# Kernel optimization log

Measured on AMD Instinct MI355X. Metric: run time of the kernel, lower is better.

The kernel has to match this reference:

```python
import jax, jax.numpy as jnp
import numpy as np

HEADS = 8
DIM_HEAD = 64
SCALE = DIM_HEAD ** -0.5


def setup_inputs() -> dict:
    key = jax.random.key(0)
    ks = jax.random.split(key, 6)
    B, S, D = 4, 2048, 512
    return {
        "hidden_states": jax.random.normal(ks[0], (B, S, D), jnp.float32),
        "Wq": jax.random.normal(ks[1], (D, D), jnp.float32) * (D ** -0.5),
        "Wk": jax.random.normal(ks[2], (D, D), jnp.float32) * (D ** -0.5),
        "Wv": jax.random.normal(ks[3], (D, D), jnp.float32) * (D ** -0.5),
        "Wo": jax.random.normal(ks[4], (D, D), jnp.float32) * (D ** -0.5),
        "bo": jnp.zeros((D,), jnp.float32),
    }


def reference(hidden_states, Wq, Wk, Wv, Wo, bo):
    B, S, D = hidden_states.shape
    H, Dh = HEADS, DIM_HEAD
    # Linear projections (torch Linear: x @ W.T; weights here stored as [D, D] used directly)
    q = hidden_states @ Wq  # [B,S,D]
    k = hidden_states @ Wk
    v = hidden_states @ Wv
    # head_to_batch_dim: [B,S,D] -> [B,H,S,Dh]
    q = q.reshape(B, S, H, Dh).transpose(0, 2, 1, 3)
    k = k.reshape(B, S, H, Dh).transpose(0, 2, 1, 3)
    v = v.reshape(B, S, H, Dh).transpose(0, 2, 1, 3)
    # scaled dot-product attention, scores materialized as in baddbmm path
    scores = jnp.einsum("bhqd,bhkd->bhqk", q, k) * SCALE  # [B,H,S,S]
    probs = jax.nn.softmax(scores, axis=-1)
    out = jnp.einsum("bhqk,bhkd->bhqd", probs, v)  # [B,H,S,Dh]
    # batch_to_head_dim: [B,H,S,Dh] -> [B,S,D]
    out = out.transpose(0, 2, 1, 3).reshape(B, S, D)
    # output projection (Dropout with p=0 is identity)
    return out @ Wo + bo
```

## Files before the change

kernel.cpp:

```cpp
#include <hip/hip_runtime.h>
#include <cstdint>
#include <cstddef>


typedef __bf16 bf16;
typedef __bf16 bf16x4_t __attribute__((ext_vector_type(4)));
typedef __bf16 bf16x8_t __attribute__((ext_vector_type(8)));
typedef float  floatx4  __attribute__((ext_vector_type(4)));
typedef short  shortx4  __attribute__((ext_vector_type(4)));
typedef uint32_t u32x4  __attribute__((ext_vector_type(4)));

#define NB   4
#define SEQ  2048
#define DM   512
#define NH   8
#define DH   64
#define MTOT (NB * SEQ)


__device__ __forceinline__ void gload16(const void* g, void* l) {
    __builtin_amdgcn_global_load_lds((const __attribute__((address_space(1))) unsigned int*)g,
                                     (__attribute__((address_space(3))) unsigned int*)l,
                                     16, 0, 0);
}

__device__ __forceinline__ shortx4 pack4(floatx4 v) {
    union { bf16x4_t h; shortx4 s; } u;
    u.h = (bf16x4_t){ (bf16)v[0], (bf16)v[1], (bf16)v[2], (bf16)v[3] };
    return u.s;
}

__global__ __launch_bounds__(256) void prep(
        const float* __restrict__ X, const float* __restrict__ Wq, const float* __restrict__ Wk,
        const float* __restrict__ Wv, const float* __restrict__ Wo,
        bf16* __restrict__ xb, bf16* __restrict__ Wqkvt, bf16* __restrict__ Wot) {
    __shared__ float T[64][65];
    const int tid = threadIdx.x;
    const int bx = blockIdx.x;
    if (bx < 4096) {
        int i = (bx * 256 + tid) * 4;
        float4 v = *(const float4*)(X + i);
        bf16x4_t o = { (bf16)v.x, (bf16)v.y, (bf16)v.z, (bf16)v.w };
        *(bf16x4_t*)(xb + i) = o;
        return;
    }
    const int idx = bx - 4096;
    const int m = idx >> 6;
    const int k0 = ((idx >> 3) & 7) * 64, n0 = (idx & 7) * 64;
    const float* W = (m == 0) ? Wq : (m == 1) ? Wk : (m == 2) ? Wv : Wo;
    const float scale = (m == 0) ? 0.18033688011112042f : 1.0f;
#pragma unroll
    for (int p = 0; p < 4; p++) {
        int row = p * 16 + (tid >> 4), col = (tid & 15) * 4;
        float4 v = *(const float4*)(W + (size_t)(k0 + row) * DM + n0 + col);
        T[row][col + 0] = v.x * scale; T[row][col + 1] = v.y * scale;
        T[row][col + 2] = v.z * scale; T[row][col + 3] = v.w * scale;
    }
    __syncthreads();
#pragma unroll
    for (int p = 0; p < 4; p++) {
        int nr = p * 16 + (tid >> 4), kc = (tid & 15) * 4;
        bf16x4_t o = { (bf16)T[kc][nr], (bf16)T[kc + 1][nr], (bf16)T[kc + 2][nr], (bf16)T[kc + 3][nr] };
        bf16* dst = (m < 3) ? (Wqkvt + ((size_t)(m * DM + n0 + nr)) * DM + k0 + kc)
                            : (Wot + (size_t)(n0 + nr) * DM + k0 + kc);
        *(bf16x4_t*)dst = o;
    }
}

__global__ __launch_bounds__(256) void gemm_qkv(
        const bf16* __restrict__ A, const bf16* __restrict__ Bt,
        bf16* __restrict__ Qh, bf16* __restrict__ Kh, bf16* __restrict__ Vt) {
    __shared__ __attribute__((aligned(16))) bf16 AB[2][2][128 * 64];
    const int tid = threadIdx.x;
    const int wave = tid >> 6, lane = tid & 63;
    const int l15 = lane & 15, quad = lane >> 4, h7 = l15 & 7;
    const int m0 = blockIdx.x * 128, n0 = blockIdx.y * 128;
    const int mw = (wave >> 1) * 64, nw = (wave & 1) * 64;
    const int srow = lane >> 3, sc = (lane & 7) ^ srow;

    auto stage = [&](int buf, int k0) {
#pragma unroll
        for (int t = 0; t < 4; t++) {
            int rb = wave * 32 + t * 8;
            gload16(A  + (size_t)(m0 + rb + srow) * DM + k0 + sc * 8, AB[buf][0] + rb * 64);
            gload16(Bt + (size_t)(n0 + rb + srow) * DM + k0 + sc * 8, AB[buf][1] + rb * 64);
        }
    };

    floatx4 zero = {0.f, 0.f, 0.f, 0.f};
    floatx4 acc[4][4];
#pragma unroll
    for (int i = 0; i < 4; i++)
#pragma unroll
        for (int j = 0; j < 4; j++) acc[i][j] = zero;

    stage(0, 0);
    for (int kt = 0; kt < DM / 64; kt++) {
        __syncthreads();
        if (kt + 1 < DM / 64) stage((kt + 1) & 1, (kt + 1) * 64);
        const bf16* As = AB[kt & 1][0];
        const bf16* Bs = AB[kt & 1][1];
#pragma unroll
        for (int ks = 0; ks < 2; ks++) {
            bf16x8_t af[4], bfr[4];
#pragma unroll
            for (int i = 0; i < 4; i++)
                af[i] = *(const bf16x8_t*)(As + (mw + i * 16 + l15) * 64 + (((ks * 4 + quad) ^ h7) * 8));
#pragma unroll
            for (int j = 0; j < 4; j++)
                bfr[j] = *(const bf16x8_t*)(Bs + (nw + j * 16 + l15) * 64 + (((ks * 4 + quad) ^ h7) * 8));
#pragma unroll
            for (int i = 0; i < 4; i++)
#pragma unroll
                for (int j = 0; j < 4; j++)
                    acc[i][j] = __builtin_amdgcn_mfma_f32_16x16x32_bf16(af[i], bfr[j], acc[i][j], 0, 0, 0);
        }
    }

    bf16* E = (bf16*)AB;
    const int sect = n0 >> 9;
    const int bq = m0 >> 11;
    __syncthreads();
    if (sect != 2) {
        bf16* dstbase = (sect == 0) ? Qh : Kh;
#pragma unroll
        for (int i = 0; i < 4; i++)
#pragma unroll
            for (int j = 0; j < 4; j++)
#pragma unroll
                for (int r = 0; r < 4; r++)
                    E[(mw + i * 16 + quad * 4 + r) * 136 + nw + j * 16 + l15] = (bf16)acc[i][j][r];
        __syncthreads();
#pragma unroll
        for (int pp = 0; pp < 8; pp++) {
            int idx = pp * 256 + tid;
            int rowl = idx >> 4, chunk = idx & 15;
            u32x4 v = *(const u32x4*)(E + rowl * 136 + chunk * 8);
            int s = (m0 + rowl) & (SEQ - 1);
            int n = n0 + chunk * 8;
            int h = (n >> 6) & 7, d = n & 63;
            *(u32x4*)(dstbase + (((size_t)(bq * NH + h)) * SEQ + s) * DH + d) = v;
        }
    } else {
#pragma unroll
        for (int i = 0; i < 4; i++)
#pragma unroll
            for (int j = 0; j < 4; j++)
                *(shortx4*)(E + (nw + j * 16 + l15) * 136 + mw + i * 16 + quad * 4) = pack4(acc[i][j]);
        __syncthreads();
#pragma unroll
        for (int pp = 0; pp < 8; pp++) {
            int idx = pp * 256 + tid;
            int rowl = idx >> 4, chunk = idx & 15;
            u32x4 v = *(const u32x4*)(E + rowl * 136 + chunk * 8);
            int n = n0 + rowl;
            int h = (n >> 6) & 7, d = n & 63;
            int s = (m0 & (SEQ - 1)) + chunk * 8;
            *(u32x4*)(Vt + (((size_t)(bq * NH + h)) * DH + d) * SEQ + s) = v;
        }
    }
}

__global__ __launch_bounds__(256) void gemm_out(
        const bf16* __restrict__ A, const bf16* __restrict__ Bt,
        const float* __restrict__ bo, float* __restrict__ out) {
    __shared__ __attribute__((aligned(16))) bf16 Ao[2][64 * 64];
    __shared__ __attribute__((aligned(16))) bf16 Bo[2][128 * 64];
    const int tid = threadIdx.x;
    const int wave = tid >> 6, lane = tid & 63;
    const int l15 = lane & 15, quad = lane >> 4, h7 = l15 & 7;
    const int m0 = blockIdx.x * 64, n0 = blockIdx.y * 128;
    const int nw = wave * 32;
    const int srow = lane >> 3, sc = (lane & 7) ^ srow;

    auto stage = [&](int buf, int k0) {
#pragma unroll
        for (int t = 0; t < 2; t++) {
            int rb = wave * 16 + t * 8;
            gload16(A + (size_t)(m0 + rb + srow) * DM + k0 + sc * 8, Ao[buf] + rb * 64);
        }
#pragma unroll
        for (int t = 0; t < 4; t++) {
            int rb = wave * 32 + t * 8;
            gload16(Bt + (size_t)(n0 + rb + srow) * DM + k0 + sc * 8, Bo[buf] + rb * 64);
        }
    };

    floatx4 zero = {0.f, 0.f, 0.f, 0.f};
    floatx4 acc[4][2];
#pragma unroll
    for (int i = 0; i < 4; i++)
#pragma unroll
        for (int j = 0; j < 2; j++) acc[i][j] = zero;

    stage(0, 0);
    for (int kt = 0; kt < DM / 64; kt++) {
        __syncthreads();
        if (kt + 1 < DM / 64) stage((kt + 1) & 1, (kt + 1) * 64);
        const bf16* As = Ao[kt & 1];
        const bf16* Bs = Bo[kt & 1];
#pragma unroll
        for (int ks = 0; ks < 2; ks++) {
            bf16x8_t af[4], bfr[2];
#pragma unroll
            for (int i = 0; i < 4; i++)
                af[i] = *(const bf16x8_t*)(As + (i * 16 + l15) * 64 + (((ks * 4 + quad) ^ h7) * 8));
#pragma unroll
            for (int j = 0; j < 2; j++)
                bfr[j] = *(const bf16x8_t*)(Bs + (nw + j * 16 + l15) * 64 + (((ks * 4 + quad) ^ h7) * 8));
#pragma unroll
            for (int i = 0; i < 4; i++)
#pragma unroll
                for (int j = 0; j < 2; j++)
                    acc[i][j] = __builtin_amdgcn_mfma_f32_16x16x32_bf16(af[i], bfr[j], acc[i][j], 0, 0, 0);
        }
    }
#pragma unroll
    for (int i = 0; i < 4; i++)
#pragma unroll
        for (int j = 0; j < 2; j++)
#pragma unroll
            for (int r = 0; r < 4; r++) {
                int m = m0 + i * 16 + quad * 4 + r;
                int n = n0 + nw + j * 16 + l15;
                out[(size_t)m * DM + n] = acc[i][j][r] + bo[n];
            }
}

__global__ __launch_bounds__(256, 2) void flash_attn(
        const bf16* __restrict__ Q, const bf16* __restrict__ Kh,
        const bf16* __restrict__ Vt, bf16* __restrict__ Ob) {
    __shared__ __attribute__((aligned(16))) bf16 SMEM[4 * 8192];
    const int tid = threadIdx.x;
    const int wave = tid >> 6, lane = tid & 63;
    const int l15 = lane & 15, quad = lane >> 4, h7 = l15 & 7;
    const int qh = wave >> 1, kvh = wave & 1;
    const int qt = blockIdx.x & 15, bh = blockIdx.x >> 4;
    const int q0 = qt * 128;
    const bf16* Kb = Kh + (size_t)bh * SEQ * DH;
    const bf16* Vb = Vt + (size_t)bh * DH * SEQ;

    bf16x8_t aq[4][2];
#pragma unroll
    for (int sub = 0; sub < 4; sub++) {
        const bf16* qr = Q + ((size_t)bh * SEQ + q0 + qh * 64 + sub * 16 + l15) * DH;
        aq[sub][0] = *(const bf16x8_t*)(qr + quad * 8);
        aq[sub][1] = *(const bf16x8_t*)(qr + 32 + quad * 8);
    }

    const int srow = lane >> 3, sc = (lane & 7) ^ srow;
    auto stage = [&](int buf, int kv0) {
#pragma unroll
        for (int t = 0; t < 2; t++) {
            int rb = wave * 16 + t * 8;
            gload16(Kb + (size_t)(kv0 + rb + srow) * DH + sc * 8, SMEM + buf * 8192 + rb * 64);
            gload16(Vb + (size_t)(rb + srow) * SEQ + kv0 + sc * 8, SMEM + buf * 8192 + 4096 + rb * 64);
        }
    };

    floatx4 zero = {0.f, 0.f, 0.f, 0.f};
    floatx4 oacc[4][4];
    float l_run[4] = {0.f, 0.f, 0.f, 0.f};
#pragma unroll
    for (int sub = 0; sub < 4; sub++)
#pragma unroll
        for (int d = 0; d < 4; d++) oacc[sub][d] = zero;

    stage(0, 0);
    stage(1, 64);
    for (int seg = 0; seg < 16; seg++) {
        __syncthreads();
        if (seg < 15) {
            stage((2 * seg + 2) & 3, (2 * seg + 2) * 64);
            stage((2 * seg + 3) & 3, (2 * seg + 3) * 64);
        }
#pragma unroll
        for (int half = 0; half < 2; half++) {
            const bf16* Ks = SMEM + ((2 * seg + half) & 3) * 8192;
            const bf16* Vs = Ks + 4096;
            floatx4 st[4][2];
#pragma unroll
            for (int nsl = 0; nsl < 2; nsl++) {
                int row = (kvh * 2 + nsl) * 16 + l15;
                const bf16* kr = Ks + row * 64;
                bf16x8_t k0 = *(const bf16x8_t*)(kr + ((quad ^ h7) * 8));
                bf16x8_t k1 = *(const bf16x8_t*)(kr + (((4 + quad) ^ h7) * 8));
#pragma unroll
                for (int sub = 0; sub < 4; sub++) {
                    floatx4 a = zero;
                    a = __builtin_amdgcn_mfma_f32_16x16x32_bf16(k0, aq[sub][0], a, 0, 0, 0);
                    a = __builtin_amdgcn_mfma_f32_16x16x32_bf16(k1, aq[sub][1], a, 0, 0, 0);
                    st[sub][nsl] = a;
                }
            }
#pragma unroll
            for (int sub = 0; sub < 4; sub++) {
                float s = 0.f;
#pragma unroll
                for (int nsl = 0; nsl < 2; nsl++)
#pragma unroll
                    for (int r = 0; r < 4; r++) {
                        float p = __builtin_amdgcn_exp2f(st[sub][nsl][r]);
                        st[sub][nsl][r] = p;
                        s += p;
                    }
                l_run[sub] += s;
            }
#pragma unroll
            for (int cl = 0; cl < 2; cl++) {
                int c = kvh * 2 + cl;
                shortx4 ap[4];
#pragma unroll
                for (int sub = 0; sub < 4; sub++) ap[sub] = pack4(st[sub][cl]);
                int cc = 2 * c + (quad >> 1);
#pragma unroll
                for (int d = 0; d < 4; d++) {
                    const bf16* vr = Vs + (d * 16 + l15) * 64;
                    shortx4 bv = *(const shortx4*)(vr + ((cc ^ h7) * 8) + (quad & 1) * 4);
#pragma unroll
                    for (int sub = 0; sub < 4; sub++)
                        oacc[sub][d] = __builtin_amdgcn_mfma_f32_16x16x16bf16_1k(ap[sub], bv, oacc[sub][d], 0, 0, 0);
                }
            }
        }
    }

    float lf[4];
#pragma unroll
    for (int sub = 0; sub < 4; sub++) {
        float l = l_run[sub];
        l += __shfl_xor(l, 16, 64);
        l += __shfl_xor(l, 32, 64);
        lf[sub] = l;
    }
    __syncthreads();
    float* blob = (float*)SMEM + qh * (68 * 64);
    if (kvh == 1) {
#pragma unroll
        for (int sub = 0; sub < 4; sub++)
#pragma unroll
            for (int d = 0; d < 4; d++)
#pragma unroll
                for (int r = 0; r < 4; r++)
                    blob[((sub * 4 + d) * 4 + r) * 64 + lane] = oacc[sub][d][r];
#pragma unroll
        for (int sub = 0; sub < 4; sub++)
            blob[(64 + sub) * 64 + lane] = lf[sub];
    }
    __syncthreads();
    if (kvh == 0) {
#pragma unroll
        for (int sub = 0; sub < 4; sub++)
#pragma unroll
            for (int d = 0; d < 4; d++)
#pragma unroll
                for (int r = 0; r < 4; r++)
                    oacc[sub][d][r] += blob[((sub * 4 + d) * 4 + r) * 64 + lane];
#pragma unroll
        for (int sub = 0; sub < 4; sub++)
            lf[sub] += blob[(64 + sub) * 64 + lane];

        const int b = bh >> 3, h = bh & 7;
#pragma unroll
        for (int sub = 0; sub < 4; sub++) {
            float linv[4];
#pragma unroll
            for (int r = 0; r < 4; r++) linv[r] = 1.0f / __shfl(lf[sub], quad * 4 + r, 64);
#pragma unroll
            for (int d = 0; d < 4; d++)
#pragma unroll
                for (int r = 0; r < 4; r++) {
                    int s = q0 + qh * 64 + sub * 16 + quad * 4 + r;
                    Ob[((size_t)b * SEQ + s) * DM + h * DH + d * 16 + l15] = (bf16)(oacc[sub][d][r] * linv[r]);
                }
        }
    }
}

extern "C" void kernel_launch(void* const* d_in, const int* in_sizes, int n_in,
                              void* d_out, int out_size, void* d_ws, size_t ws_size,
                              hipStream_t stream) {
    const float* X  = (const float*)d_in[0];
    const float* Wq = (const float*)d_in[1];
    const float* Wk = (const float*)d_in[2];
    const float* Wv = (const float*)d_in[3];
    const float* Wo = (const float*)d_in[4];
    const float* bo = (const float*)d_in[5];
    float* out = (float*)d_out;

    char* ws = (char*)d_ws;
    bf16* Xb    = (bf16*)(ws + 0);
    bf16* Wqkvt = (bf16*)(ws + 8388608);
    bf16* Wot   = (bf16*)(ws + 9961472);
    bf16* Qh    = (bf16*)(ws + 10485760);
    bf16* Kh    = (bf16*)(ws + 18874368);
    bf16* Vt    = (bf16*)(ws + 27262976);
    bf16* Ob    = (bf16*)(ws + 35651584);

    prep<<<4096 + 256, 256, 0, stream>>>(X, Wq, Wk, Wv, Wo, Xb, Wqkvt, Wot);
    gemm_qkv<<<dim3(MTOT / 128, 1536 / 128), 256, 0, stream>>>(Xb, Wqkvt, Qh, Kh, Vt);
    flash_attn<<<NB * NH * (SEQ / 128), 256, 0, stream>>>(Qh, Kh, Vt, Ob);
    gemm_out<<<dim3(MTOT / 64, DM / 128), 256, 0, stream>>>(Ob, Wot, bo, out);
}
```

Before: 148.8 us.

## Shrink QKV GEMM k-tile to 32 and remap attention block indexing

```diff
diff --git a/kernel.cpp b/kernel.cpp
--- a/kernel.cpp
+++ b/kernel.cpp
@@ -70,20 +70,25 @@
 __global__ __launch_bounds__(256) void gemm_qkv(
         const bf16* __restrict__ A, const bf16* __restrict__ Bt,
         bf16* __restrict__ Qh, bf16* __restrict__ Kh, bf16* __restrict__ Vt) {
-    __shared__ __attribute__((aligned(16))) bf16 AB[2][2][128 * 64];
+    __shared__ __attribute__((aligned(16))) bf16 SM[128 * 136];
     const int tid = threadIdx.x;
     const int wave = tid >> 6, lane = tid & 63;
-    const int l15 = lane & 15, quad = lane >> 4, h7 = l15 & 7;
+    const int l15 = lane & 15, quad = lane >> 4;
+    const int sw = (l15 >> 1) & 3;
     const int m0 = blockIdx.x * 128, n0 = blockIdx.y * 128;
     const int mw = (wave >> 1) * 64, nw = (wave & 1) * 64;
-    const int srow = lane >> 3, sc = (lane & 7) ^ srow;
+    const int srow2 = lane >> 2;
 
     auto stage = [&](int buf, int k0) {
-#pragma unroll
-        for (int t = 0; t < 4; t++) {
-            int rb = wave * 32 + t * 8;
-            gload16(A  + (size_t)(m0 + rb + srow) * DM + k0 + sc * 8, AB[buf][0] + rb * 64);
-            gload16(Bt + (size_t)(n0 + rb + srow) * DM + k0 + sc * 8, AB[buf][1] + rb * 64);
+        bf16* Ad = SM + buf * 8192;
+        bf16* Bd = SM + buf * 8192 + 4096;
+#pragma unroll
+        for (int t = 0; t < 2; t++) {
+            int rbase = t * 64 + 16 * wave;
+            int row = rbase + srow2;
+            int g = (lane & 3) ^ ((row >> 1) & 3);
+            gload16(A  + (size_t)(m0 + row) * DM + k0 + g * 8, Ad + rbase * 32);
+            gload16(Bt + (size_t)(n0 + row) * DM + k0 + g * 8, Bd + rbase * 32);
         }
     };
 
@@ -95,29 +100,26 @@
         for (int j = 0; j < 4; j++) acc[i][j] = zero;
 
     stage(0, 0);
-    for (int kt = 0; kt < DM / 64; kt++) {
+    for (int kt = 0; kt < DM / 32; kt++) {
         __syncthreads();
-        if (kt + 1 < DM / 64) stage((kt + 1) & 1, (kt + 1) * 64);
-        const bf16* As = AB[kt & 1][0];
-        const bf16* Bs = AB[kt & 1][1];
-#pragma unroll
-        for (int ks = 0; ks < 2; ks++) {
-            bf16x8_t af[4], bfr[4];
-#pragma unroll
-            for (int i = 0; i < 4; i++)
-                af[i] = *(const bf16x8_t*)(As + (mw + i * 16 + l15) * 64 + (((ks * 4 + quad) ^ h7) * 8));
+        if (kt + 1 < DM / 32) stage((kt + 1) & 1, (kt + 1) * 32);
+        const bf16* As = SM + (kt & 1) * 8192;
+        const bf16* Bs = As + 4096;
+        bf16x8_t af[4], bfr[4];
+#pragma unroll
+        for (int i = 0; i < 4; i++)
+            af[i] = *(const bf16x8_t*)(As + (mw + i * 16 + l15) * 32 + ((quad ^ sw) * 8));
+#pragma unroll
+        for (int j = 0; j < 4; j++)
+            bfr[j] = *(const bf16x8_t*)(Bs + (nw + j * 16 + l15) * 32 + ((quad ^ sw) * 8));
+#pragma unroll
+        for (int i = 0; i < 4; i++)
 #pragma unroll
             for (int j = 0; j < 4; j++)
-                bfr[j] = *(const bf16x8_t*)(Bs + (nw + j * 16 + l15) * 64 + (((ks * 4 + quad) ^ h7) * 8));
-#pragma unroll
-            for (int i = 0; i < 4; i++)
-#pragma unroll
-                for (int j = 0; j < 4; j++)
-                    acc[i][j] = __builtin_amdgcn_mfma_f32_16x16x32_bf16(af[i], bfr[j], acc[i][j], 0, 0, 0);
-        }
-    }
-
-    bf16* E = (bf16*)AB;
+                acc[i][j] = __builtin_amdgcn_mfma_f32_16x16x32_bf16(af[i], bfr[j], acc[i][j], 0, 0, 0);
+    }
+
+    bf16* E = SM;
     const int sect = n0 >> 9;
     const int bq = m0 >> 11;
     __syncthreads();
@@ -177,12 +179,12 @@
 #pragma unroll
         for (int t = 0; t < 2; t++) {
             int rb = wave * 16 + t * 8;
-            gload16(A + (size_t)(m0 + rb + srow) * DM + k0 + sc * 8, Ao[buf] + rb * 64);
+            gload16(A + (size_t)(m0 + rb + srow) * DM + k0 + sc * 8, &Ao[buf][rb * 64]);
         }
 #pragma unroll
         for (int t = 0; t < 4; t++) {
             int rb = wave * 32 + t * 8;
-            gload16(Bt + (size_t)(n0 + rb + srow) * DM + k0 + sc * 8, Bo[buf] + rb * 64);
+            gload16(Bt + (size_t)(n0 + rb + srow) * DM + k0 + sc * 8, &Bo[buf][rb * 64]);
         }
     };
 
@@ -197,8 +199,8 @@
     for (int kt = 0; kt < DM / 64; kt++) {
         __syncthreads();
         if (kt + 1 < DM / 64) stage((kt + 1) & 1, (kt + 1) * 64);
-        const bf16* As = Ao[kt & 1];
-        const bf16* Bs = Bo[kt & 1];
+        const bf16* As = &Ao[kt & 1][0];
+        const bf16* Bs = &Bo[kt & 1][0];
 #pragma unroll
         for (int ks = 0; ks < 2; ks++) {
             bf16x8_t af[4], bfr[2];
@@ -235,7 +237,9 @@
     const int wave = tid >> 6, lane = tid & 63;
     const int l15 = lane & 15, quad = lane >> 4, h7 = l15 & 7;
     const int qh = wave >> 1, kvh = wave & 1;
-    const int qt = blockIdx.x & 15, bh = blockIdx.x >> 4;
+    const int bx = blockIdx.x;
+    const int qt = (bx >> 3) & 15;
+    const int bh = (bx & 7) | ((bx >> 7) << 3);
     const int q0 = qt * 128;
     const bf16* Kb = Kh + (size_t)bh * SEQ * DH;
     const bf16* Vb = Vt + (size_t)bh * DH * SEQ;
```

Result: no change. 150.9 us (+1.4%).
